# Performance work log

Measured on AMD Instinct MI355X. Metric: run time of the kernel, lower is better.

Reference implementation:

```python
import jax, jax.numpy as jnp
import numpy as np


def setup_inputs() -> dict:
    key = jax.random.key(0)
    kq, kk, kv = jax.random.split(key, 3)
    B, H, S, D = 1, 16, 4096, 64
    q = jax.random.normal(kq, (B, H, S, D), dtype=jnp.float32)
    k = jax.random.normal(kk, (B, H, S, D), dtype=jnp.float32)
    v = jax.random.normal(kv, (B, H, S, D), dtype=jnp.float32)
    return {"q": q, "k": k, "v": v}


def reference(q, k, v):
    # softmax(q @ k^T * d^-0.5 + causal_bias) @ v
    S = q.shape[-2]
    scale = q.shape[-1] ** -0.5
    logits = jnp.einsum("bhqd,bhkd->bhqk", q, k) * scale  # [B,H,S,S]
    causal = jnp.tril(jnp.ones((S, S), dtype=bool))  # additive bias: 0 allowed, -inf future
    logits = jnp.where(causal, logits, -jnp.inf)
    probs = jax.nn.softmax(logits, axis=-1)
    return jnp.einsum("bhqk,bhkd->bhqd", probs, v)
```

## Files before the change

### kernel.cpp

```cpp
#include <hip/hip_runtime.h>
#include <hip/hip_bf16.h>
#include <math.h>

typedef __attribute__((ext_vector_type(8))) short short8;
typedef __attribute__((ext_vector_type(4))) short short4v;
typedef __attribute__((ext_vector_type(4))) float f32x4;

#define S_LEN 4096
#define D_DIM 64
#define QBLK 64
#define NHEAD 16
#define QSCALE (0.125f * 1.44269504088896340736f)
#define NEG_BIG (-3.0e38f)
#define DEFER_THR 8.0f

__device__ __forceinline__ short f2bf(float f) {
  union { float f; unsigned u; } x;
  x.f = f;
  unsigned r = x.u + 0x7FFFu + ((x.u >> 16) & 1u);
  return (short)(r >> 16);
}

__device__ __forceinline__ unsigned cvtpk_bf16(float lo, float hi) {
  unsigned r;
  asm("v_cvt_pk_bf16_f32 %0, %1, %2" : "=v"(r) : "v"(lo), "v"(hi));
  return r;
}

__device__ __forceinline__ float f3max(float a, float b, float c) {
  return fmaxf(fmaxf(a, b), c);
}

__device__ __forceinline__ void gload_lds16(const void* g, void* l) {
  __builtin_amdgcn_global_load_lds(
      (const __attribute__((address_space(1))) unsigned*)g,
      (__attribute__((address_space(3))) unsigned*)l, 16, 0, 0);
}

__global__ __launch_bounds__(256) void conv_kv(
    const float* __restrict__ K, const float* __restrict__ V,
    short* __restrict__ Kb, short* __restrict__ Vt) {
  const int h = blockIdx.y;
  const int s0 = blockIdx.x * 64;
  const int tid = threadIdx.x;
  __shared__ short vt[64][68];
  const float* kp = K + ((size_t)h * S_LEN + s0) * D_DIM;
  const float* vp = V + ((size_t)h * S_LEN + s0) * D_DIM;
  short* kb = Kb + ((size_t)h * S_LEN + s0) * D_DIM;
#pragma unroll
  for (int p = 0; p < 4; ++p) {
    const int idx = tid + (p << 8);
    const int row = idx >> 4, c4 = (idx & 15) << 2;
    const float4 kf = *(const float4*)(kp + row * D_DIM + c4);
    short4v ks;
    ks[0] = f2bf(kf.x); ks[1] = f2bf(kf.y); ks[2] = f2bf(kf.z); ks[3] = f2bf(kf.w);
    *(short4v*)(kb + row * D_DIM + c4) = ks;
    const float4 vf = *(const float4*)(vp + row * D_DIM + c4);
    short4v vs;
    vs[0] = f2bf(vf.x); vs[1] = f2bf(vf.y); vs[2] = f2bf(vf.z); vs[3] = f2bf(vf.w);
    *(short4v*)&vt[row][c4] = vs;
  }
  __syncthreads();
  short* vo = Vt + ((size_t)h * D_DIM) * S_LEN + s0;
#pragma unroll
  for (int p = 0; p < 4; ++p) {
    const int idx = tid + (p << 8);
    const int d = idx >> 4, sc = (idx & 15) << 2;
    short4v x;
    x[0] = vt[sc + 0][d]; x[1] = vt[sc + 1][d];
    x[2] = vt[sc + 2][d]; x[3] = vt[sc + 3][d];
    *(short4v*)(vo + (size_t)d * S_LEN + sc) = x;
  }
}

__global__ __launch_bounds__(256, 4) void attn_fwd(
    const float* __restrict__ Q, const short* __restrict__ Kb,
    const short* __restrict__ Vt, float* __restrict__ O) {
  const int lid = blockIdx.x;
  const int xcd = lid & 7, slot = lid >> 3;
  const int h = xcd * 2 + (slot & 1);
  const int pr = slot >> 1;

  const int tid = threadIdx.x;
  const int w = tid >> 6, l = tid & 63, g = l >> 4, c = l & 15;

  __shared__ __align__(16) char SMEM[40960];
  short* K0 = (short*)SMEM;
  short* V0 = (short*)(SMEM + 16384);
  short* P0 = (short*)(SMEM + 32768);

  const float* Qh = Q + ((size_t)h * S_LEN) * D_DIM;
  const char* Kh = (const char*)(Kb + ((size_t)h * S_LEN) * D_DIM);
  const char* Vh = (const char*)(Vt + ((size_t)h * D_DIM) * S_LEN);
  float* Oh = O + ((size_t)h * S_LEN) * D_DIM;

  auto stage = [&](int t, int b) {
    const char* kg = Kh + (size_t)(64 * t) * 128;
    const char* vg = Vh + 128 * t;
#pragma unroll
    for (int i = 0; i < 2; ++i) {
      const int q = w * 2 + i;
      const int r = q * 8 + (l >> 3);
      const int ch = l & 7;
      const int swz = (ch ^ (r & 7)) << 4;
      gload_lds16(kg + (size_t)r * 128 + swz, K0 + b * 4096 + q * 512);
      gload_lds16(vg + (size_t)r * (S_LEN * 2) + swz, V0 + b * 4096 + q * 512);
    }
  };

  for (int rep = 0; rep < 2; ++rep) {
    const int a = rep ? (63 - pr) : pr;
    const int qb0 = a * QBLK;
    const int q0 = qb0 + w * 16;
    const int qg = q0 + c;

    if (rep) __syncthreads();
    stage(0, 0);

    short8 qf[2];
    {
      const float* qp = Qh + (size_t)qg * D_DIM;
#pragma unroll
      for (int hh = 0; hh < 2; ++hh) {
        short8 aa;
#pragma unroll
        for (int j = 0; j < 8; ++j) aa[j] = f2bf(qp[hh * 32 + g * 8 + j] * QSCALE);
        qf[hh] = aa;
      }
    }

    f32x4 o[4];
#pragma unroll
    for (int i = 0; i < 4; ++i) o[i] = (f32x4)0.f;
    float m_r = 0.f, l_r = 0.f;

    __syncthreads();
    int cur = 0;

    for (int t = 0; t <= a; ++t) {
      if (t < a) stage(t + 1, cur ^ 1);
      const short* Kl = K0 + cur * 4096;
      const short* Vl = V0 + cur * 4096;

      const float negm = -m_r;
      f32x4 s[4];
      __builtin_amdgcn_s_setprio(1);
#pragma unroll
      for (int sub = 0; sub < 4; ++sub) {
        const int kvr = sub * 16 + c;
        f32x4 acc = (f32x4)negm;
#pragma unroll
        for (int hh = 0; hh < 2; ++hh) {
          const int idx = (kvr * 64 + hh * 32 + g * 8) ^ ((c & 7) << 3);
          acc = __builtin_amdgcn_mfma_f32_16x16x32_bf16(
              *(const short8*)&Kl[idx], qf[hh], acc, 0, 0, 0);
        }
        s[sub] = acc;
      }
      __builtin_amdgcn_s_setprio(0);

      if (64 * t + 63 > q0) {
        const int thr = qg - 64 * t - 4 * g;
#pragma unroll
        for (int sub = 0; sub < 4; ++sub)
#pragma unroll
          for (int r = 0; r < 4; ++r)
            if (16 * sub + r > thr) s[sub][r] = NEG_BIG;
      }

      float t0 = f3max(s[0][0], s[0][1], s[0][2]);
      float t1 = f3max(s[0][3], s[1][0], s[1][1]);
      float t2 = f3max(s[1][2], s[1][3], s[2][0]);
      float t3 = f3max(s[2][1], s[2][2], s[2][3]);
      float t4 = f3max(s[3][0], s[3][1], s[3][2]);
      float pm = fmaxf(f3max(t0, t1, t2), f3max(t3, t4, s[3][3]));
      pm = fmaxf(pm, __shfl_xor(pm, 16));
      pm = fmaxf(pm, __shfl_xor(pm, 32));
      if (__any(pm > DEFER_THR)) {
        const float d = fmaxf(pm, 0.f);
        const float al = __builtin_amdgcn_exp2f(-d);
        m_r += d;
        l_r *= al;
#pragma unroll
        for (int dt = 0; dt < 4; ++dt)
#pragma unroll
          for (int r = 0; r < 4; ++r) o[dt][r] *= al;
#pragma unroll
        for (int sub = 0; sub < 4; ++sub)
#pragma unroll
          for (int r = 0; r < 4; ++r) s[sub][r] -= d;
      }
      float rs = 0.f;
#pragma unroll
      for (int sub = 0; sub < 4; ++sub)
#pragma unroll
        for (int r = 0; r < 4; ++r) {
          s[sub][r] = __builtin_amdgcn_exp2f(s[sub][r]);
          rs += s[sub][r];
        }
      l_r += rs;

      short* Pw = P0 + w * 1024;
#pragma unroll
      for (int sub = 0; sub < 4; ++sub) {
        const unsigned u0 = cvtpk_bf16(s[sub][0], s[sub][1]);
        const unsigned u1 = cvtpk_bf16(s[sub][2], s[sub][3]);
        const unsigned long long uu = ((unsigned long long)u1 << 32) | u0;
        const int idx = (c * 64 + sub * 16 + g * 4) ^ ((c & 7) << 3);
        *(unsigned long long*)&Pw[idx] = uu;
      }
      short8 pf[2];
#pragma unroll
      for (int hk = 0; hk < 2; ++hk) {
        const int idx = (c * 64 + hk * 32 + g * 8) ^ ((c & 7) << 3);
        pf[hk] = *(const short8*)&Pw[idx];
      }
      __builtin_amdgcn_s_setprio(1);
#pragma unroll
      for (int dt = 0; dt < 4; ++dt) {
        const int dr = dt * 16 + c;
#pragma unroll
        for (int hk = 0; hk < 2; ++hk) {
          const int idx = (dr * 64 + hk * 32 + g * 8) ^ ((c & 7) << 3);
          o[dt] = __builtin_amdgcn_mfma_f32_16x16x32_bf16(
              *(const short8*)&Vl[idx], pf[hk], o[dt], 0, 0, 0);
        }
      }
      __builtin_amdgcn_s_setprio(0);

      __syncthreads();
      cur ^= 1;
    }

    float lsum = l_r;
    lsum += __shfl_xor(lsum, 16);
    lsum += __shfl_xor(lsum, 32);
    const float inv = 1.f / lsum;
    float* scr = (float*)SMEM + w * (16 * 68);
#pragma unroll
    for (int dt = 0; dt < 4; ++dt)
#pragma unroll
      for (int r = 0; r < 4; ++r)
        scr[c * 68 + dt * 16 + g * 4 + r] = o[dt][r] * inv;
    const int q_l = l >> 2, prt = l & 3;
    const float* sr = scr + q_l * 68 + prt * 16;
    float* op = Oh + (size_t)(q0 + q_l) * D_DIM + prt * 16;
#pragma unroll
    for (int k = 0; k < 4; ++k) *(f32x4*)(op + k * 4) = *(const f32x4*)(sr + k * 4);
  }
}

extern "C" void kernel_launch(void* const* d_in, const int* in_sizes, int n_in,
                              void* d_out, int out_size, void* d_ws, size_t ws_size,
                              hipStream_t stream) {
  const float* q = (const float*)d_in[0];
  const float* k = (const float*)d_in[1];
  const float* v = (const float*)d_in[2];
  float* out = (float*)d_out;
  short* kb = (short*)d_ws;
  short* vt = kb + (size_t)NHEAD * S_LEN * D_DIM;
  dim3 cgrid(S_LEN / 64, NHEAD);
  conv_kv<<<cgrid, dim3(256), 0, stream>>>(k, v, kb, vt);
  attn_fwd<<<dim3(512), dim3(256), 0, stream>>>(q, kb, vt, out);
}
```

Before: 82.16 us.

## Split KV tiles across two wave groups per block and merge partial softmax

Each block now runs 512 threads split into two groups of four waves. Both groups handle the same query rows but take alternating KV tiles, each with its own double-buffered K/V LDS region. At the end the partial outputs, row sums and running maxima are merged through LDS with rescaling. This is meant to shorten each block's serial KV loop and raise the number of waves per CU. In exchange, LDS use doubles to 80KB, and the launch bounds of 512 threads with 4 blocks may force a tight VGPR budget and spills. The two groups can also be unbalanced by one tile, and the merge adds an extra barrier.

New measurement: 76.39 us. 1.08x faster.

```diff
diff --git a/kernel.cpp b/kernel.cpp
--- a/kernel.cpp
+++ b/kernel.cpp
@@ -73,7 +73,7 @@
   }
 }
 
-__global__ __launch_bounds__(256, 4) void attn_fwd(
+__global__ __launch_bounds__(512, 4) void attn_fwd(
     const float* __restrict__ Q, const short* __restrict__ Kb,
     const short* __restrict__ Vt, float* __restrict__ O) {
   const int lid = blockIdx.x;
@@ -82,40 +82,45 @@
   const int pr = slot >> 1;
 
   const int tid = threadIdx.x;
-  const int w = tid >> 6, l = tid & 63, g = l >> 4, c = l & 15;
-
-  __shared__ __align__(16) char SMEM[40960];
-  short* K0 = (short*)SMEM;
-  short* V0 = (short*)(SMEM + 16384);
-  short* P0 = (short*)(SMEM + 32768);
+  const int w = tid >> 6;
+  const int grp = w >> 2;
+  const int wq = w & 3;
+  const int l = tid & 63, g = l >> 4, c = l & 15;
+
+  __shared__ __align__(16) char SMEM[81920];
+  short* Kg = (short*)SMEM + grp * 8192;
+  short* Vg = (short*)(SMEM + 32768) + grp * 8192;
+  short* P0 = (short*)(SMEM + 65536);
 
   const float* Qh = Q + ((size_t)h * S_LEN) * D_DIM;
   const char* Kh = (const char*)(Kb + ((size_t)h * S_LEN) * D_DIM);
   const char* Vh = (const char*)(Vt + ((size_t)h * D_DIM) * S_LEN);
   float* Oh = O + ((size_t)h * S_LEN) * D_DIM;
 
-  auto stage = [&](int t, int b) {
-    const char* kg = Kh + (size_t)(64 * t) * 128;
-    const char* vg = Vh + 128 * t;
+  auto stage = [&](int tg, int b) {
+    const char* kg = Kh + (size_t)(64 * tg) * 128;
+    const char* vg = Vh + 128 * tg;
 #pragma unroll
     for (int i = 0; i < 2; ++i) {
-      const int q = w * 2 + i;
-      const int r = q * 8 + (l >> 3);
+      const int qr = wq * 2 + i;
+      const int r = qr * 8 + (l >> 3);
       const int ch = l & 7;
       const int swz = (ch ^ (r & 7)) << 4;
-      gload_lds16(kg + (size_t)r * 128 + swz, K0 + b * 4096 + q * 512);
-      gload_lds16(vg + (size_t)r * (S_LEN * 2) + swz, V0 + b * 4096 + q * 512);
+      gload_lds16(kg + (size_t)r * 128 + swz, Kg + b * 4096 + qr * 512);
+      gload_lds16(vg + (size_t)r * (S_LEN * 2) + swz, Vg + b * 4096 + qr * 512);
     }
   };
 
   for (int rep = 0; rep < 2; ++rep) {
     const int a = rep ? (63 - pr) : pr;
     const int qb0 = a * QBLK;
-    const int q0 = qb0 + w * 16;
+    const int q0 = qb0 + wq * 16;
     const int qg = q0 + c;
+    const int nmax = (a >> 1) + 1;
+    const int nloc = (a >= grp) ? (((a - grp) >> 1) + 1) : 0;
 
     if (rep) __syncthreads();
-    stage(0, 0);
+    if (nloc > 0) stage(grp, 0);
 
     short8 qf[2];
     {
@@ -137,116 +142,139 @@
     __syncthreads();
     int cur = 0;
 
-    for (int t = 0; t <= a; ++t) {
-      if (t < a) stage(t + 1, cur ^ 1);
-      const short* Kl = K0 + cur * 4096;
-      const short* Vl = V0 + cur * 4096;
-
-      const float negm = -m_r;
-      f32x4 s[4];
-      __builtin_amdgcn_s_setprio(1);
-#pragma unroll
-      for (int sub = 0; sub < 4; ++sub) {
-        const int kvr = sub * 16 + c;
-        f32x4 acc = (f32x4)negm;
-#pragma unroll
-        for (int hh = 0; hh < 2; ++hh) {
-          const int idx = (kvr * 64 + hh * 32 + g * 8) ^ ((c & 7) << 3);
-          acc = __builtin_amdgcn_mfma_f32_16x16x32_bf16(
-              *(const short8*)&Kl[idx], qf[hh], acc, 0, 0, 0);
-        }
-        s[sub] = acc;
+    for (int tl = 0; tl < nmax; ++tl) {
+      const int tg = 2 * tl + grp;
+      if (tl + 1 < nloc) stage(tg + 2, cur ^ 1);
+      if (tl < nloc) {
+        const short* Kl = Kg + cur * 4096;
+        const short* Vl = Vg + cur * 4096;
+
+        const float negm = -m_r;
+        f32x4 s[4];
+        __builtin_amdgcn_s_setprio(1);
+#pragma unroll
+        for (int sub = 0; sub < 4; ++sub) {
+          const int kvr = sub * 16 + c;
+          f32x4 acc = (f32x4)negm;
+#pragma unroll
+          for (int hh = 0; hh < 2; ++hh) {
+            const int idx = (kvr * 64 + hh * 32 + g * 8) ^ ((c & 7) << 3);
+            acc = __builtin_amdgcn_mfma_f32_16x16x32_bf16(
+                *(const short8*)&Kl[idx], qf[hh], acc, 0, 0, 0);
+          }
+          s[sub] = acc;
+        }
+        __builtin_amdgcn_s_setprio(0);
+
+        if (64 * tg + 63 > q0) {
+          const int thr = qg - 64 * tg - 4 * g;
+#pragma unroll
+          for (int sub = 0; sub < 4; ++sub)
+#pragma unroll
+            for (int r = 0; r < 4; ++r)
+              if (16 * sub + r > thr) s[sub][r] = NEG_BIG;
+        }
+
+        float t0 = f3max(s[0][0], s[0][1], s[0][2]);
+        float t1 = f3max(s[0][3], s[1][0], s[1][1]);
+        float t2 = f3max(s[1][2], s[1][3], s[2][0]);
+        float t3 = f3max(s[2][1], s[2][2], s[2][3]);
+        float t4 = f3max(s[3][0], s[3][1], s[3][2]);
+        float pm = fmaxf(f3max(t0, t1, t2), f3max(t3, t4, s[3][3]));
+        pm = fmaxf(pm, __shfl_xor(pm, 16));
+        pm = fmaxf(pm, __shfl_xor(pm, 32));
+        if (__any(pm > DEFER_THR)) {
+          const float d = fmaxf(pm, 0.f);
+          const float al = __builtin_amdgcn_exp2f(-d);
+          m_r += d;
+          l_r *= al;
+#pragma unroll
+          for (int dt = 0; dt < 4; ++dt)
+#pragma unroll
+            for (int r = 0; r < 4; ++r) o[dt][r] *= al;
+#pragma unroll
+          for (int sub = 0; sub < 4; ++sub)
+#pragma unroll
+            for (int r = 0; r < 4; ++r) s[sub][r] -= d;
+        }
+        float rs = 0.f;
+#pragma unroll
+        for (int sub = 0; sub < 4; ++sub)
+#pragma unroll
+          for (int r = 0; r < 4; ++r) {
+            s[sub][r] = __builtin_amdgcn_exp2f(s[sub][r]);
+            rs += s[sub][r];
+          }
+        l_r += rs;
+
+        short* Pw = P0 + w * 1024;
+#pragma unroll
+        for (int sub = 0; sub < 4; ++sub) {
+          const unsigned u0 = cvtpk_bf16(s[sub][0], s[sub][1]);
+          const unsigned u1 = cvtpk_bf16(s[sub][2], s[sub][3]);
+          const unsigned long long uu = ((unsigned long long)u1 << 32) | u0;
+          const int idx = (c * 64 + sub * 16 + g * 4) ^ ((c & 7) << 3);
+          *(unsigned long long*)&Pw[idx] = uu;
+        }
+        short8 pf[2];
+#pragma unroll
+        for (int hk = 0; hk < 2; ++hk) {
+          const int idx = (c * 64 + hk * 32 + g * 8) ^ ((c & 7) << 3);
+          pf[hk] = *(const short8*)&Pw[idx];
+        }
+        __builtin_amdgcn_s_setprio(1);
+#pragma unroll
+        for (int dt = 0; dt < 4; ++dt) {
+          const int dr = dt * 16 + c;
+#pragma unroll
+          for (int hk = 0; hk < 2; ++hk) {
+            const int idx = (dr * 64 + hk * 32 + g * 8) ^ ((c & 7) << 3);
+            o[dt] = __builtin_amdgcn_mfma_f32_16x16x32_bf16(
+                *(const short8*)&Vl[idx], pf[hk], o[dt], 0, 0, 0);
+          }
+        }
+        __builtin_amdgcn_s_setprio(0);
       }
-      __builtin_amdgcn_s_setprio(0);
-
-      if (64 * t + 63 > q0) {
-        const int thr = qg - 64 * t - 4 * g;
-#pragma unroll
-        for (int sub = 0; sub < 4; ++sub)
-#pragma unroll
-          for (int r = 0; r < 4; ++r)
-            if (16 * sub + r > thr) s[sub][r] = NEG_BIG;
-      }
-
-      float t0 = f3max(s[0][0], s[0][1], s[0][2]);
-      float t1 = f3max(s[0][3], s[1][0], s[1][1]);
-      float t2 = f3max(s[1][2], s[1][3], s[2][0]);
-      float t3 = f3max(s[2][1], s[2][2], s[2][3]);
-      float t4 = f3max(s[3][0], s[3][1], s[3][2]);
-      float pm = fmaxf(f3max(t0, t1, t2), f3max(t3, t4, s[3][3]));
-      pm = fmaxf(pm, __shfl_xor(pm, 16));
-      pm = fmaxf(pm, __shfl_xor(pm, 32));
-      if (__any(pm > DEFER_THR)) {
-        const float d = fmaxf(pm, 0.f);
-        const float al = __builtin_amdgcn_exp2f(-d);
-        m_r += d;
-        l_r *= al;
-#pragma unroll
-        for (int dt = 0; dt < 4; ++dt)
-#pragma unroll
-          for (int r = 0; r < 4; ++r) o[dt][r] *= al;
-#pragma unroll
-        for (int sub = 0; sub < 4; ++sub)
-#pragma unroll
-          for (int r = 0; r < 4; ++r) s[sub][r] -= d;
-      }
-      float rs = 0.f;
-#pragma unroll
-      for (int sub = 0; sub < 4; ++sub)
-#pragma unroll
-        for (int r = 0; r < 4; ++r) {
-          s[sub][r] = __builtin_amdgcn_exp2f(s[sub][r]);
-          rs += s[sub][r];
-        }
-      l_r += rs;
-
-      short* Pw = P0 + w * 1024;
-#pragma unroll
-      for (int sub = 0; sub < 4; ++sub) {
-        const unsigned u0 = cvtpk_bf16(s[sub][0], s[sub][1]);
-        const unsigned u1 = cvtpk_bf16(s[sub][2], s[sub][3]);
-        const unsigned long long uu = ((unsigned long long)u1 << 32) | u0;
-        const int idx = (c * 64 + sub * 16 + g * 4) ^ ((c & 7) << 3);
-        *(unsigned long long*)&Pw[idx] = uu;
-      }
-      short8 pf[2];
-#pragma unroll
-      for (int hk = 0; hk < 2; ++hk) {
-        const int idx = (c * 64 + hk * 32 + g * 8) ^ ((c & 7) << 3);
-        pf[hk] = *(const short8*)&Pw[idx];
-      }
-      __builtin_amdgcn_s_setprio(1);
-#pragma unroll
-      for (int dt = 0; dt < 4; ++dt) {
-        const int dr = dt * 16 + c;
-#pragma unroll
-        for (int hk = 0; hk < 2; ++hk) {
-          const int idx = (dr * 64 + hk * 32 + g * 8) ^ ((c & 7) << 3);
-          o[dt] = __builtin_amdgcn_mfma_f32_16x16x32_bf16(
-              *(const short8*)&Vl[idx], pf[hk], o[dt], 0, 0, 0);
-        }
-      }
-      __builtin_amdgcn_s_setprio(0);
 
       __syncthreads();
       cur ^= 1;
     }
 
-    float lsum = l_r;
-    lsum += __shfl_xor(lsum, 16);
-    lsum += __shfl_xor(lsum, 32);
-    const float inv = 1.f / lsum;
-    float* scr = (float*)SMEM + w * (16 * 68);
-#pragma unroll
-    for (int dt = 0; dt < 4; ++dt)
-#pragma unroll
-      for (int r = 0; r < 4; ++r)
-        scr[c * 68 + dt * 16 + g * 4 + r] = o[dt][r] * inv;
-    const int q_l = l >> 2, prt = l & 3;
-    const float* sr = scr + q_l * 68 + prt * 16;
-    float* op = Oh + (size_t)(q0 + q_l) * D_DIM + prt * 16;
-#pragma unroll
-    for (int k = 0; k < 4; ++k) *(f32x4*)(op + k * 4) = *(const f32x4*)(sr + k * 4);
+    float* mrg = (float*)(SMEM + 32768) + wq * 1152;
+    if (grp == 1) {
+#pragma unroll
+      for (int dt = 0; dt < 4; ++dt)
+#pragma unroll
+        for (int r = 0; r < 4; ++r) mrg[(dt * 4 + r) * 64 + l] = o[dt][r];
+      mrg[1024 + l] = l_r;
+      mrg[1088 + l] = m_r;
+    }
+    __syncthreads();
+    if (grp == 0) {
+      const float m1 = mrg[1088 + l];
+      const float l1 = mrg[1024 + l];
+      const float M = fmaxf(m_r, m1);
+      const float a0 = __builtin_amdgcn_exp2f(m_r - M);
+      const float a1 = __builtin_amdgcn_exp2f(m1 - M);
+      float lm = l_r * a0 + l1 * a1;
+      lm += __shfl_xor(lm, 16);
+      lm += __shfl_xor(lm, 32);
+      const float inv = 1.f / lm;
+      float* scr = (float*)SMEM + wq * (16 * 68);
+#pragma unroll
+      for (int dt = 0; dt < 4; ++dt)
+#pragma unroll
+        for (int r = 0; r < 4; ++r) {
+          const float om = o[dt][r] * a0 + mrg[(dt * 4 + r) * 64 + l] * a1;
+          scr[c * 68 + dt * 16 + g * 4 + r] = om * inv;
+        }
+      const int q_l = l >> 2, prt = l & 3;
+      const float* sr = scr + q_l * 68 + prt * 16;
+      float* op = Oh + (size_t)(q0 + q_l) * D_DIM + prt * 16;
+#pragma unroll
+      for (int k2 = 0; k2 < 4; ++k2)
+        *(f32x4*)(op + k2 * 4) = *(const f32x4*)(sr + k2 * 4);
+    }
   }
 }
 
@@ -261,5 +289,5 @@
   short* vt = kb + (size_t)NHEAD * S_LEN * D_DIM;
   dim3 cgrid(S_LEN / 64, NHEAD);
   conv_kv<<<cgrid, dim3(256), 0, stream>>>(k, v, kb, vt);
-  attn_fwd<<<dim3(512), dim3(256), 0, stream>>>(q, kb, vt, out);
-}
+  attn_fwd<<<dim3(512), dim3(512), 0, stream>>>(q, kb, vt, out);
+}
```
